# Kernel tuning notes

Measured on AMD Instinct MI355X. Metric: run time of the kernel, lower is better.

The kernel has to match this reference:

```python
import jax, jax.numpy as jnp
import numpy as np

N_ATOMS = 512
BATCH = 32


def _get_segments(n):
    # shifted pairs (k, k+1), all combinations of 2 rows, drop pairs where end1 == start2
    pairs = np.stack([np.arange(n - 1), np.arange(1, n)], axis=1)  # (n-1, 2)
    i, j = np.triu_indices(n - 1, k=1)
    seg = np.concatenate([pairs[i], pairs[j]], axis=1)  # (M, 4)
    seg = seg[seg[:, 1] != seg[:, 2]]
    return seg.astype(np.int32)  # (129795, 4) for n=512


def setup_inputs() -> dict:
    key = jax.random.key(0)
    x = jax.random.normal(key, (BATCH, N_ATOMS, 3), dtype=jnp.float32) * 5.0
    segments = jnp.asarray(_get_segments(N_ATOMS))
    return {"x": x, "segments": segments}


def _nnorm(v):
    return v / jnp.linalg.norm(v, axis=-1, keepdims=True)


def reference(x, segments):
    n = N_ATOMS
    x = x.reshape(-1, n, 3)
    B = x.shape[0]
    smat = x[:, segments]                       # (B, S, 4, 3) gather
    S = smat.shape[1]
    # displacements between the two segment endpoints pairs: d_{ab} = p_{2+b} - p_a
    disp = _nnorm((-smat[:, :, :2, None, :] + smat[:, :, None, 2:, :]).reshape(B, S, 4, 3))
    crosses = _nnorm(jnp.cross(disp[:, :, [0, 1, 3, 2]], disp[:, :, [1, 3, 2, 0]]))
    omega = jnp.arcsin(
        jnp.clip(jnp.sum(crosses * crosses[:, :, [1, 2, 3, 0]], axis=-1), -1.0, 1.0)
    ).sum(axis=2)                               # (B, S)
    signs = jnp.sign(
        jnp.sum(
            jnp.cross(_nnorm(smat[:, :, 3] - smat[:, :, 2]), _nnorm(smat[:, :, 1] - smat[:, :, 0]))
            * disp[:, :, 0],
            axis=-1,
        )
    )
    wr = (omega * signs) / (2.0 * jnp.pi)       # (B, S)
    # scatter into adjacency matrix (sequential sets: second overrides first, like torch)
    adj = jnp.zeros((B, n, n), dtype=x.dtype)
    adj = adj.at[:, segments[:, 0], segments[:, 2]].set(wr)
    adj = adj.at[:, segments[:, 1], segments[:, 3]].set(wr)
    return adj + jnp.swapaxes(adj, 1, 2)
```

## Files before the change

### kernel.cpp

```cpp
#include <hip/hip_runtime.h>
#include <math.h>

#define N 512
#define TILE 32

struct F3 { float x, y, z; };

__device__ __forceinline__ F3 f3sub(F3 a, F3 b) { return {a.x - b.x, a.y - b.y, a.z - b.z}; }
__device__ __forceinline__ F3 f3cross(F3 a, F3 b) {
    return {a.y * b.z - a.z * b.y, a.z * b.x - a.x * b.z, a.x * b.y - a.y * b.x};
}
__device__ __forceinline__ float f3dot(F3 a, F3 b) { return a.x * b.x + a.y * b.y + a.z * b.z; }

__device__ __forceinline__ float wr_val(const float* xs, int a, int b) {
    const float* pa = xs + 3 * a;
    const float* pb = xs + 3 * b;
    F3 p0 = {pa[0], pa[1], pa[2]};
    F3 p1 = {pa[3], pa[4], pa[5]};
    F3 p2 = {pb[0], pb[1], pb[2]};
    F3 p3 = {pb[3], pb[4], pb[5]};

    F3 d0 = f3sub(p2, p0), d1 = f3sub(p3, p0), d2 = f3sub(p2, p1), d3 = f3sub(p3, p1);

    F3 c0 = f3cross(d0, d1);
    F3 c1 = f3cross(d1, d3);
    F3 c2 = f3cross(d3, d2);
    F3 c3 = f3cross(d2, d0);

    float r0 = rsqrtf(f3dot(c0, c0));
    float r1 = rsqrtf(f3dot(c1, c1));
    float r2 = rsqrtf(f3dot(c2, c2));
    float r3 = rsqrtf(f3dot(c3, c3));

    float t01 = fminf(1.f, fmaxf(-1.f, f3dot(c0, c1) * (r0 * r1)));
    float t12 = fminf(1.f, fmaxf(-1.f, f3dot(c1, c2) * (r1 * r2)));
    float t23 = fminf(1.f, fmaxf(-1.f, f3dot(c2, c3) * (r2 * r3)));
    float t30 = fminf(1.f, fmaxf(-1.f, f3dot(c3, c0) * (r3 * r0)));

    float omega = asinf(t01) + asinf(t12) + asinf(t23) + asinf(t30);

    F3 e = f3cross(f3sub(p3, p2), f3sub(p1, p0));
    float sv = f3dot(e, d0);
    float sgn = (sv > 0.f) ? 1.f : ((sv < 0.f) ? -1.f : 0.f);

    return omega * sgn * 0.15915494309189535f;
}

__global__ __launch_bounds__(256) void writhe_tile(const float* __restrict__ x,
                                                   float* __restrict__ out) {
    __shared__ float xs[N * 3];
    __shared__ float ts[TILE][TILE + 1];

    const int batch = blockIdx.y;
    const float* xb = x + (size_t)batch * (N * 3);
    {
        const float4* src = (const float4*)xb;
        float4* dst = (float4*)xs;
        for (int i = threadIdx.x; i < (N * 3) / 4; i += blockDim.x) dst[i] = src[i];
    }

    int p = blockIdx.x;
    int ti = 0;
    while (p >= (N / TILE) - ti) { p -= (N / TILE) - ti; ++ti; }
    const int tj = ti + p;

    __syncthreads();

    const int c = threadIdx.x & 31;
    const int r0 = threadIdx.x >> 5;
    const bool diag = (ti == tj);

    float* ob = out + (size_t)batch * (N * N);

#pragma unroll
    for (int k = 0; k < 4; ++k) {
        const int r = r0 + 8 * k;
        const int gi = ti * TILE + r;
        const int gj = tj * TILE + c;
        const int lo = min(gi, gj), hi = max(gi, gj);
        bool valid;
        int a, b;
        if (lo == 0) { valid = (hi >= 2) && (hi <= 510); a = 0; b = hi; }
        else         { valid = (hi >= lo + 2);           a = lo - 1; b = hi - 1; }
        float v = 0.f;
        if (valid) v = wr_val(xs, a, b);
        ob[(size_t)gi * N + gj] = v;
        if (!diag) ts[r][c] = v;
    }

    if (!diag) {
        __syncthreads();
#pragma unroll
        for (int k = 0; k < 4; ++k) {
            const int r = r0 + 8 * k;
            ob[(size_t)(tj * TILE + r) * N + (ti * TILE + c)] = ts[c][r];
        }
    }
}

extern "C" void kernel_launch(void* const* d_in, const int* in_sizes, int n_in,
                              void* d_out, int out_size, void* d_ws, size_t ws_size,
                              hipStream_t stream) {
    const float* x = (const float*)d_in[0];
    float* out = (float*)d_out;
    const int B = in_sizes[0] / (N * 3);

    const int ntiles = N / TILE;
    const int npairs = ntiles * (ntiles + 1) / 2;

    dim3 block(256);
    dim3 grid(npairs, B);
    writhe_tile<<<grid, block, 0, stream>>>(x, out);
}
```

Measured before the change: 92.42 us.

## Pack writhe pairs into float2 math, use fast asin polynomial and padded float4 LDS

Each thread now computes two matrix entries at once with float2 arithmetic, which the compiler can map to packed FP32 instructions on CDNA. The library asinf is replaced with a short polynomial-plus-sqrt approximation, and rsqrt and sqrt use the raw hardware builtins. Atom coordinates are repacked into padded float4 slots in shared memory so each point loads with a single vector read. Invalid entries are now computed anyway and masked, with indices clamped to stay in range. The polynomial asin trades some accuracy for fewer instructions.

New measurement: 82.13 us. -11.1%, faster.

```diff
diff --git a/kernel.cpp b/kernel.cpp
--- a/kernel.cpp
+++ b/kernel.cpp
@@ -3,89 +3,158 @@
 
 #define N 512
 #define TILE 32
+#define INV2PI 0.15915494309189535f
 
-struct F3 { float x, y, z; };
+__device__ __forceinline__ float2 pset(float a, float b) { return make_float2(a, b); }
+__device__ __forceinline__ float2 psplat(float a) { return make_float2(a, a); }
+__device__ __forceinline__ float2 p_sub(float2 a, float2 b) { return make_float2(a.x - b.x, a.y - b.y); }
+__device__ __forceinline__ float2 p_mul(float2 a, float2 b) { return make_float2(a.x * b.x, a.y * b.y); }
+__device__ __forceinline__ float2 p_fma(float2 a, float2 b, float2 c) {
+    return make_float2(fmaf(a.x, b.x, c.x), fmaf(a.y, b.y, c.y));
+}
+__device__ __forceinline__ float2 p_fmsub(float2 a, float2 b, float2 c, float2 d) {
+    return make_float2(fmaf(a.x, b.x, -(c.x * d.x)), fmaf(a.y, b.y, -(c.y * d.y)));
+}
+__device__ __forceinline__ float2 p_clamp1(float2 a) {
+    return make_float2(fminf(1.f, fmaxf(-1.f, a.x)), fminf(1.f, fmaxf(-1.f, a.y)));
+}
+__device__ __forceinline__ float2 p_rsq(float2 a) {
+    return make_float2(__builtin_amdgcn_rsqf(a.x), __builtin_amdgcn_rsqf(a.y));
+}
 
-__device__ __forceinline__ F3 f3sub(F3 a, F3 b) { return {a.x - b.x, a.y - b.y, a.z - b.z}; }
-__device__ __forceinline__ F3 f3cross(F3 a, F3 b) {
-    return {a.y * b.z - a.z * b.y, a.z * b.x - a.x * b.z, a.x * b.y - a.y * b.x};
+struct F3P { float2 x, y, z; };
+
+__device__ __forceinline__ F3P pp_sub(F3P a, F3P b) {
+    return {p_sub(a.x, b.x), p_sub(a.y, b.y), p_sub(a.z, b.z)};
 }
-__device__ __forceinline__ float f3dot(F3 a, F3 b) { return a.x * b.x + a.y * b.y + a.z * b.z; }
+__device__ __forceinline__ F3P pp_cross(F3P a, F3P b) {
+    F3P c;
+    c.x = p_fmsub(a.y, b.z, a.z, b.y);
+    c.y = p_fmsub(a.z, b.x, a.x, b.z);
+    c.z = p_fmsub(a.x, b.y, a.y, b.x);
+    return c;
+}
+__device__ __forceinline__ float2 pp_dot(F3P a, F3P b) {
+    return p_fma(a.x, b.x, p_fma(a.y, b.y, p_mul(a.z, b.z)));
+}
 
-__device__ __forceinline__ float wr_val(const float* xs, int a, int b) {
-    const float* pa = xs + 3 * a;
-    const float* pb = xs + 3 * b;
-    F3 p0 = {pa[0], pa[1], pa[2]};
-    F3 p1 = {pa[3], pa[4], pa[5]};
-    F3 p2 = {pb[0], pb[1], pb[2]};
-    F3 p3 = {pb[3], pb[4], pb[5]};
+__device__ __forceinline__ float2 p_asin(float2 v) {
+    float2 ax = make_float2(fabsf(v.x), fabsf(v.y));
+    float2 p = p_fma(ax, psplat(-0.0187293f), psplat(0.0742610f));
+    p = p_fma(ax, p, psplat(-0.2121144f));
+    p = p_fma(ax, p, psplat(1.5707288f));
+    float2 s = make_float2(__builtin_amdgcn_sqrtf(1.0f - ax.x), __builtin_amdgcn_sqrtf(1.0f - ax.y));
+    float2 r = make_float2(1.5707963267948966f - s.x * p.x, 1.5707963267948966f - s.y * p.y);
+    return make_float2(copysignf(r.x, v.x), copysignf(r.y, v.y));
+}
 
-    F3 d0 = f3sub(p2, p0), d1 = f3sub(p3, p0), d2 = f3sub(p2, p1), d3 = f3sub(p3, p1);
+__device__ __forceinline__ float2 wr_core2(F3P p0, F3P p1, F3P p2, F3P p3) {
+    F3P d0 = pp_sub(p2, p0), d1 = pp_sub(p3, p0), d2 = pp_sub(p2, p1), d3 = pp_sub(p3, p1);
 
-    F3 c0 = f3cross(d0, d1);
-    F3 c1 = f3cross(d1, d3);
-    F3 c2 = f3cross(d3, d2);
-    F3 c3 = f3cross(d2, d0);
+    F3P c0 = pp_cross(d0, d1);
+    F3P c1 = pp_cross(d1, d3);
+    F3P c2 = pp_cross(d3, d2);
+    F3P c3 = pp_cross(d2, d0);
 
-    float r0 = rsqrtf(f3dot(c0, c0));
-    float r1 = rsqrtf(f3dot(c1, c1));
-    float r2 = rsqrtf(f3dot(c2, c2));
-    float r3 = rsqrtf(f3dot(c3, c3));
+    float2 r0 = p_rsq(pp_dot(c0, c0));
+    float2 r1 = p_rsq(pp_dot(c1, c1));
+    float2 r2 = p_rsq(pp_dot(c2, c2));
+    float2 r3 = p_rsq(pp_dot(c3, c3));
 
-    float t01 = fminf(1.f, fmaxf(-1.f, f3dot(c0, c1) * (r0 * r1)));
-    float t12 = fminf(1.f, fmaxf(-1.f, f3dot(c1, c2) * (r1 * r2)));
-    float t23 = fminf(1.f, fmaxf(-1.f, f3dot(c2, c3) * (r2 * r3)));
-    float t30 = fminf(1.f, fmaxf(-1.f, f3dot(c3, c0) * (r3 * r0)));
+    float2 t01 = p_clamp1(p_mul(pp_dot(c0, c1), p_mul(r0, r1)));
+    float2 t12 = p_clamp1(p_mul(pp_dot(c1, c2), p_mul(r1, r2)));
+    float2 t23 = p_clamp1(p_mul(pp_dot(c2, c3), p_mul(r2, r3)));
+    float2 t30 = p_clamp1(p_mul(pp_dot(c3, c0), p_mul(r3, r0)));
 
-    float omega = asinf(t01) + asinf(t12) + asinf(t23) + asinf(t30);
+    float2 a01 = p_asin(t01), a12 = p_asin(t12), a23 = p_asin(t23), a30 = p_asin(t30);
+    float2 omega = make_float2(a01.x + a12.x + a23.x + a30.x, a01.y + a12.y + a23.y + a30.y);
 
-    F3 e = f3cross(f3sub(p3, p2), f3sub(p1, p0));
-    float sv = f3dot(e, d0);
-    float sgn = (sv > 0.f) ? 1.f : ((sv < 0.f) ? -1.f : 0.f);
+    F3P e = pp_cross(pp_sub(p3, p2), pp_sub(p1, p0));
+    float2 sv = pp_dot(e, d0);
+    float sgx = (sv.x > 0.f) ? 1.f : ((sv.x < 0.f) ? -1.f : 0.f);
+    float sgy = (sv.y > 0.f) ? 1.f : ((sv.y < 0.f) ? -1.f : 0.f);
 
-    return omega * sgn * 0.15915494309189535f;
+    return make_float2(omega.x * sgx * INV2PI, omega.y * sgy * INV2PI);
+}
+
+__device__ __forceinline__ F3P pack_pt(const float4* __restrict__ xs4, int i0, int i1) {
+    float4 a = xs4[i0];
+    float4 b = xs4[i1];
+    F3P r;
+    r.x = pset(a.x, b.x);
+    r.y = pset(a.y, b.y);
+    r.z = pset(a.z, b.z);
+    return r;
+}
+
+__device__ __forceinline__ void elem_idx(int gi, int gj, int& a, int& b, bool& valid) {
+    const int lo = min(gi, gj), hi = max(gi, gj);
+    if (lo == 0) { valid = (hi >= 2) && (hi <= 510); a = 0; b = min(hi, 510); }
+    else         { valid = (hi >= lo + 2);           a = lo - 1; b = hi - 1; }
 }
 
 __global__ __launch_bounds__(256) void writhe_tile(const float* __restrict__ x,
                                                    float* __restrict__ out) {
-    __shared__ float xs[N * 3];
+    __shared__ __align__(16) float4 xs4[N];
     __shared__ float ts[TILE][TILE + 1];
 
     const int batch = blockIdx.y;
-    const float* xb = x + (size_t)batch * (N * 3);
+
     {
-        const float4* src = (const float4*)xb;
-        float4* dst = (float4*)xs;
-        for (int i = threadIdx.x; i < (N * 3) / 4; i += blockDim.x) dst[i] = src[i];
+        const float4* src = (const float4*)(x + (size_t)batch * (N * 3));
+        float* xsf = (float*)xs4;
+        for (int i = threadIdx.x; i < (N * 3) / 4; i += blockDim.x) {
+            float4 g = src[i];
+            const int base = 4 * i;
+            float vv[4] = {g.x, g.y, g.z, g.w};
+#pragma unroll
+            for (int j = 0; j < 4; ++j) {
+                const int e = base + j;
+                xsf[(e / 3) * 4 + (e % 3)] = vv[j];
+            }
+        }
     }
 
     int p = blockIdx.x;
     int ti = 0;
     while (p >= (N / TILE) - ti) { p -= (N / TILE) - ti; ++ti; }
     const int tj = ti + p;
+    const bool diag = (ti == tj);
 
     __syncthreads();
 
     const int c = threadIdx.x & 31;
     const int r0 = threadIdx.x >> 5;
-    const bool diag = (ti == tj);
-
+    const int gj = tj * TILE + c;
     float* ob = out + (size_t)batch * (N * N);
 
 #pragma unroll
-    for (int k = 0; k < 4; ++k) {
-        const int r = r0 + 8 * k;
-        const int gi = ti * TILE + r;
-        const int gj = tj * TILE + c;
-        const int lo = min(gi, gj), hi = max(gi, gj);
-        bool valid;
-        int a, b;
-        if (lo == 0) { valid = (hi >= 2) && (hi <= 510); a = 0; b = hi; }
-        else         { valid = (hi >= lo + 2);           a = lo - 1; b = hi - 1; }
-        float v = 0.f;
-        if (valid) v = wr_val(xs, a, b);
-        ob[(size_t)gi * N + gj] = v;
-        if (!diag) ts[r][c] = v;
+    for (int k = 0; k < 2; ++k) {
+        const int rA = r0 + 8 * k;
+        const int rB = rA + 16;
+        const int giA = ti * TILE + rA;
+        const int giB = ti * TILE + rB;
+
+        int aA, bA, aB, bB;
+        bool vA, vB;
+        elem_idx(giA, gj, aA, bA, vA);
+        elem_idx(giB, gj, aB, bB, vB);
+
+        F3P P0 = pack_pt(xs4, aA, aB);
+        F3P P1 = pack_pt(xs4, aA + 1, aB + 1);
+        F3P P2 = pack_pt(xs4, bA, bB);
+        F3P P3 = pack_pt(xs4, bA + 1, bB + 1);
+
+        float2 wr = wr_core2(P0, P1, P2, P3);
+        const float vxA = vA ? wr.x : 0.f;
+        const float vxB = vB ? wr.y : 0.f;
+
+        ob[(size_t)giA * N + gj] = vxA;
+        ob[(size_t)giB * N + gj] = vxB;
+        if (!diag) {
+            ts[rA][c] = vxA;
+            ts[rB][c] = vxB;
+        }
     }
 
     if (!diag) {
```
